# Performance work log

Measured on AMD Instinct MI355X. Metric: run time of the kernel, lower is better.

The kernel has to match this reference:

```python
import jax, jax.numpy as jnp
import numpy as np

B, SEQ, ST, DIN, DK, DV = 2, 4096, 128, 1024, 64, 64
T = SEQ + 2 * ST  # 4352, divisible by 8 -> no pad branch in original


def _l2norm(t):
    # matches torch F.normalize(p=2, dim=-1, eps=1e-12)
    return t / jnp.maximum(jnp.linalg.norm(t, axis=-1, keepdims=True), 1e-12)


def setup_inputs() -> dict:
    key = jax.random.key(0)
    ks = jax.random.split(key, 9)
    x = jax.random.normal(ks[0], (B, T, DIN), dtype=jnp.float32)
    w = 0.02
    Wq = jax.random.normal(ks[1], (DK, DIN), dtype=jnp.float32) * w
    Wk = jax.random.normal(ks[2], (DK, DIN), dtype=jnp.float32) * w
    Wv = jax.random.normal(ks[3], (DV, DIN), dtype=jnp.float32) * w
    Wq_s = jax.random.normal(ks[4], (DK, DIN), dtype=jnp.float32) * w
    Wk_s = jax.random.normal(ks[5], (DK, DIN), dtype=jnp.float32) * w
    Wv_s = jax.random.normal(ks[6], (DV, DIN), dtype=jnp.float32) * w
    cope_emb = jax.random.normal(ks[7], (DK, T), dtype=jnp.float32)  # (1, dim_key, seq_len+2*state_len) squeezed
    scale = jnp.array([0.125], dtype=jnp.float32)  # learnable scaling_factor param
    return {"x": x, "Wq": Wq, "Wk": Wk, "Wv": Wv, "Wq_s": Wq_s,
            "Wk_s": Wk_s, "Wv_s": Wv_s, "cope_emb": cope_emb, "scale": scale}


def reference(x, Wq, Wk, Wv, Wq_s, Wk_s, Wv_s, cope_emb, scale):
    # extract_state: start-state, sequence, end-state
    xs, xm, xe = x[:, :ST], x[:, ST:ST + SEQ], x[:, ST + SEQ:]
    # project (Linear, no bias) then L2-normalize each token vector
    q = jnp.concatenate([_l2norm(xs @ Wq_s.T), _l2norm(xm @ Wq.T), _l2norm(xe @ Wq_s.T)], axis=1)
    k = jnp.concatenate([_l2norm(xs @ Wk_s.T), _l2norm(xm @ Wk.T), _l2norm(xe @ Wk_s.T)], axis=1)
    v = jnp.concatenate([_l2norm(xs @ Wv_s.T), _l2norm(xm @ Wv.T), _l2norm(xe @ Wv_s.T)], axis=1)

    # q@k^T is used both for CoPE gates and (scaled) attention scores
    logits = jnp.einsum('btd,bsd->bts', q, k)  # (B, T, T)

    # --- CoPE bias ---
    gates = jax.nn.sigmoid(logits)
    pos = jnp.cumsum(gates[:, :, ::-1], axis=-1)[:, :, ::-1]  # flip-cumsum-flip
    pos = jnp.minimum(pos, jnp.float32(T - 1))
    pos_floor = jnp.floor(pos)
    pos_ceil = jnp.ceil(pos)
    w = pos - pos_floor
    logits_int = jnp.einsum('btd,dl->btl', q, cope_emb)  # (B, T, T)
    lc = jnp.take_along_axis(logits_int, pos_ceil.astype(jnp.int32), axis=-1)
    lf = jnp.take_along_axis(logits_int, pos_floor.astype(jnp.int32), axis=-1)
    cope_bias = lc * w + lf * (1.0 - w)

    # --- causal + state-token mask: tril, with end-state rows blocked from start-state cols ---
    i = jnp.arange(T)
    mask = i[:, None] >= i[None, :]
    blocked = (i[:, None] >= SEQ + ST) & (i[None, :] < ST)
    mask = mask & (~blocked)
    attn_bias = jnp.where(mask, 0.0, -jnp.inf)[None, :, :]

    scores = logits * scale[0] + attn_bias + cope_bias
    att = jax.nn.softmax(scores, axis=-1) @ v  # (B, T, DV)
    return att
```

## Files before the change

kernel.cpp:

```cpp
#include <hip/hip_runtime.h>
#include <math.h>

#define B_ 2
#define SEQ_ 4096
#define ST_ 128
#define T_ 4352
#define DIN_ 1024
#define NW 16
#define LMAX 3328
#define LPAD 3336
#define NSLICE 272
#define SLPAD 273
#define NROW 8704

typedef _Float16 f16;
typedef __attribute__((ext_vector_type(8))) _Float16 f16x8;
typedef __attribute__((ext_vector_type(4))) float f32x4;

#define OB_WH  0
#define OB_WL  786432
#define OB_QH  1572864
#define OB_QL  2686976
#define OB_KH  3801088
#define OB_KL  4915200
#define OB_VT  6029312
#define OB_CPT 7143424
#define OB_SS  7569408
#define OB_XH  17039360
#define OB_XL  34865152
#define NEED_NEW 52690944ull

#define WT4_OFF 0
#define Q_OFF   393216
#define KT_OFF  950272
#define V_OFF   1507328

__device__ __forceinline__ int wuid() {
  return __builtin_amdgcn_readfirstlane((int)(threadIdx.x >> 6));
}

template<int CTRL, int RM>
__device__ __forceinline__ float dppadd(float x) {
  int y = __builtin_amdgcn_update_dpp(0, __float_as_int(x), CTRL, RM, 0xf, true);
  return x + __int_as_float(y);
}
__device__ __forceinline__ float wave_iscan(float x) {
  x = dppadd<0x111, 0xf>(x);
  x = dppadd<0x112, 0xf>(x);
  x = dppadd<0x114, 0xf>(x);
  x = dppadd<0x118, 0xf>(x);
  x = dppadd<0x142, 0xa>(x);
  x = dppadd<0x143, 0xc>(x);
  return x;
}
__device__ __forceinline__ float p16scan(float x) {
  x = dppadd<0x111, 0xf>(x);
  x = dppadd<0x112, 0xf>(x);
  x = dppadd<0x114, 0xf>(x);
  x = dppadd<0x118, 0xf>(x);
  return x;
}
__device__ __forceinline__ float swz15(float x) {
  return __int_as_float(__builtin_amdgcn_ds_swizzle(__float_as_int(x), 0x1F0));
}

__global__ __launch_bounds__(256) void wsplit_kernel(
    const float* __restrict__ Wq,  const float* __restrict__ Wk,
    const float* __restrict__ Wv,  const float* __restrict__ Wqs,
    const float* __restrict__ Wks, const float* __restrict__ Wvs,
    f16* __restrict__ wh, f16* __restrict__ wl) {
  const int m = blockIdx.y;
  const float* src = (m==0)?Wq:(m==1)?Wqs:(m==2)?Wk:(m==3)?Wks:(m==4)?Wv:Wvs;
  const int g0 = (int)blockIdx.x * 4096 + (int)threadIdx.x * 16;
  const float4* s4 = reinterpret_cast<const float4*>(src + g0);
  float4 v0 = s4[0], v1 = s4[1], v2 = s4[2], v3 = s4[3];
  f16x8 h0, h1, l0, l1;
  h0[0]=(f16)v0.x; h0[1]=(f16)v0.y; h0[2]=(f16)v0.z; h0[3]=(f16)v0.w;
  h0[4]=(f16)v1.x; h0[5]=(f16)v1.y; h0[6]=(f16)v1.z; h0[7]=(f16)v1.w;
  h1[0]=(f16)v2.x; h1[1]=(f16)v2.y; h1[2]=(f16)v2.z; h1[3]=(f16)v2.w;
  h1[4]=(f16)v3.x; h1[5]=(f16)v3.y; h1[6]=(f16)v3.z; h1[7]=(f16)v3.w;
  l0[0]=(f16)(v0.x-(float)h0[0]); l0[1]=(f16)(v0.y-(float)h0[1]);
  l0[2]=(f16)(v0.z-(float)h0[2]); l0[3]=(f16)(v0.w-(float)h0[3]);
  l0[4]=(f16)(v1.x-(float)h0[4]); l0[5]=(f16)(v1.y-(float)h0[5]);
  l0[6]=(f16)(v1.z-(float)h0[6]); l0[7]=(f16)(v1.w-(float)h0[7]);
  l1[0]=(f16)(v2.x-(float)h1[0]); l1[1]=(f16)(v2.y-(float)h1[1]);
  l1[2]=(f16)(v2.z-(float)h1[2]); l1[3]=(f16)(v2.w-(float)h1[3]);
  l1[4]=(f16)(v3.x-(float)h1[4]); l1[5]=(f16)(v3.y-(float)h1[5]);
  l1[6]=(f16)(v3.z-(float)h1[6]); l1[7]=(f16)(v3.w-(float)h1[7]);
  const size_t o = (size_t)m * 65536 + g0;
  *reinterpret_cast<f16x8*>(wh + o) = h0;
  *reinterpret_cast<f16x8*>(wh + o + 8) = h1;
  *reinterpret_cast<f16x8*>(wl + o) = l0;
  *reinterpret_cast<f16x8*>(wl + o + 8) = l1;
}

__global__ __launch_bounds__(256) void xsplit_kernel(
    const float* __restrict__ x, f16* __restrict__ xh, f16* __restrict__ xl) {
  const size_t g0 = ((size_t)blockIdx.x * 256 + threadIdx.x) * 16;
  const float4* s4 = reinterpret_cast<const float4*>(x + g0);
  float4 v0 = s4[0], v1 = s4[1], v2 = s4[2], v3 = s4[3];
  f16x8 h0, h1, l0, l1;
  h0[0]=(f16)v0.x; h0[1]=(f16)v0.y; h0[2]=(f16)v0.z; h0[3]=(f16)v0.w;
  h0[4]=(f16)v1.x; h0[5]=(f16)v1.y; h0[6]=(f16)v1.z; h0[7]=(f16)v1.w;
  h1[0]=(f16)v2.x; h1[1]=(f16)v2.y; h1[2]=(f16)v2.z; h1[3]=(f16)v2.w;
  h1[4]=(f16)v3.x; h1[5]=(f16)v3.y; h1[6]=(f16)v3.z; h1[7]=(f16)v3.w;
  l0[0]=(f16)(v0.x-(float)h0[0]); l0[1]=(f16)(v0.y-(float)h0[1]);
  l0[2]=(f16)(v0.z-(float)h0[2]); l0[3]=(f16)(v0.w-(float)h0[3]);
  l0[4]=(f16)(v1.x-(float)h0[4]); l0[5]=(f16)(v1.y-(float)h0[5]);
  l0[6]=(f16)(v1.z-(float)h0[6]); l0[7]=(f16)(v1.w-(float)h0[7]);
  l1[0]=(f16)(v2.x-(float)h1[0]); l1[1]=(f16)(v2.y-(float)h1[1]);
  l1[2]=(f16)(v2.z-(float)h1[2]); l1[3]=(f16)(v2.w-(float)h1[3]);
  l1[4]=(f16)(v3.x-(float)h1[4]); l1[5]=(f16)(v3.y-(float)h1[5]);
  l1[6]=(f16)(v3.z-(float)h1[6]); l1[7]=(f16)(v3.w-(float)h1[7]);
  *reinterpret_cast<f16x8*>(xh + g0) = h0;
  *reinterpret_cast<f16x8*>(xh + g0 + 8) = h1;
  *reinterpret_cast<f16x8*>(xl + g0) = l0;
  *reinterpret_cast<f16x8*>(xl + g0 + 8) = l1;
}

__global__ __launch_bounds__(256) void copet_kernel(
    const float* __restrict__ cope, f16* __restrict__ copeT) {
  __shared__ float t2[64][65];
  const int l0 = blockIdx.x << 6;
  const int tid = (int)threadIdx.x;
  #pragma unroll
  for (int p = 0; p < 16; ++p) {
    int d = (p << 2) + (tid >> 6), c = tid & 63;
    t2[d][c] = cope[(size_t)d * T_ + l0 + c];
  }
  __syncthreads();
  #pragma unroll
  for (int p = 0; p < 16; ++p) {
    int l = (p << 2) + (tid >> 6), d = tid & 63;
    copeT[(size_t)(l0 + l) * 64 + d] = (f16)t2[d][l];
  }
}

#define PM_MFMA(ACC, WHP, WLP) { \
  f16x8 bh_ = *reinterpret_cast<const f16x8*>((WHP) + (st << 5)); \
  f16x8 bl_ = *reinterpret_cast<const f16x8*>((WLP) + (st << 5)); \
  ACC = __builtin_amdgcn_mfma_f32_16x16x32_f16(xh_, bh_, ACC, 0, 0, 0); \
  ACC = __builtin_amdgcn_mfma_f32_16x16x32_f16(xl_, bh_, ACC, 0, 0, 0); \
  ACC = __builtin_amdgcn_mfma_f32_16x16x32_f16(xh_, bl_, ACC, 0, 0, 0); }

#define PM_RED(ACC, P) { \
  float s0_ = ACC[0]*ACC[0], s1_ = ACC[1]*ACC[1], s2_ = ACC[2]*ACC[2], s3_ = ACC[3]*ACC[3]; \
  s0_ += __shfl_xor(s0_, 1, 64); s1_ += __shfl_xor(s1_, 1, 64); \
  s2_ += __shfl_xor(s2_, 1, 64); s3_ += __shfl_xor(s3_, 1, 64); \
  s0_ += __shfl_xor(s0_, 2, 64); s1_ += __shfl_xor(s1_, 2, 64); \
  s2_ += __shfl_xor(s2_, 2, 64); s3_ += __shfl_xor(s3_, 2, 64); \
  s0_ += __shfl_xor(s0_, 4, 64); s1_ += __shfl_xor(s1_, 4, 64); \
  s2_ += __shfl_xor(s2_, 4, 64); s3_ += __shfl_xor(s3_, 4, 64); \
  s0_ += __shfl_xor(s0_, 8, 64); s1_ += __shfl_xor(s1_, 8, 64); \
  s2_ += __shfl_xor(s2_, 8, 64); s3_ += __shfl_xor(s3_, 8, 64); \
  if (qlo == 0) { \
    ssq[wn][P][(qhi << 2) + 0] = s0_; ssq[wn][P][(qhi << 2) + 1] = s1_; \
    ssq[wn][P][(qhi << 2) + 2] = s2_; ssq[wn][P][(qhi << 2) + 3] = s3_; } }

#define PM_QK1(ACC, P, HH, LL, RG) { \
  float tt_ = ssq[0][P][(qhi << 2) + RG] + ssq[1][P][(qhi << 2) + RG] \
            + ssq[2][P][(qhi << 2) + RG] + ssq[3][P][(qhi << 2) + RG]; \
  float rn_ = 1.f / fmaxf(sqrtf(tt_), 1e-12f); \
  float v_ = ACC[RG] * rn_; \
  f16 h_ = (f16)v_; \
  size_t ad_ = (size_t)(bt0 + (qhi << 2) + RG) * 64 + (wn << 4) + qlo; \
  HH[ad_] = h_; LL[ad_] = (f16)(v_ - (float)h_); }

#define PM_V1(ACC, P, RG) { \
  float tt_ = ssq[0][P][(qhi << 2) + RG] + ssq[1][P][(qhi << 2) + RG] \
            + ssq[2][P][(qhi << 2) + RG] + ssq[3][P][(qhi << 2) + RG]; \
  float rn_ = 1.f / fmaxf(sqrtf(tt_), 1e-12f); \
  vt[(size_t)(b * 64 + (wn << 4) + qlo) * T_ + t0 + (qhi << 2) + RG] = (f16)(ACC[RG] * rn_); }

__global__ __launch_bounds__(512, 4) void projM_kernel(
    const f16* __restrict__ xh, const f16* __restrict__ xl,
    const f16* __restrict__ wh, const f16* __restrict__ wl,
    f16* __restrict__ qh, f16* __restrict__ ql,
    f16* __restrict__ kh, f16* __restrict__ kl,
    f16* __restrict__ vt) {
  __shared__ float ssq[4][3][16];
  __shared__ float part[4][64][12];
  const int lane = (int)threadIdx.x & 63;
  const int w = wuid();
  const int wn = w & 3;
  const int kh2 = w >> 2;
  const int qlo = lane & 15, qhi = lane >> 4;
  const int bt0 = (int)blockIdx.x << 4;
  const int b = bt0 / T_;
  const int t0 = bt0 - b * T_;
  const int spec = (t0 < ST_ || t0 >= ST_ + SEQ_) ? 1 : 0;

  const int kof = kh2 << 9;
  const f16* xhr = xh + (size_t)(bt0 + qlo) * DIN_ + kof + (qhi << 3);
  const f16* xlr = xl + (size_t)(bt0 + qlo) * DIN_ + kof + (qhi << 3);
  const size_t wrow = (size_t)((wn << 4) + qlo) * 1024 + kof + (qhi << 3);
  const f16* wq  = wh + (size_t)(0 + spec) * 65536 + wrow;
  const f16* wqL = wl + (size_t)(0 + spec) * 65536 + wrow;
  const f16* wk  = wh + (size_t)(2 + spec) * 65536 + wrow;
  const f16* wkL = wl + (size_t)(2 + spec) * 65536 + wrow;
  const f16* wv  = wh + (size_t)(4 + spec) * 65536 + wrow;
  const f16* wvL = wl + (size_t)(4 + spec) * 65536 + wrow;

  f32x4 aq = {0.f,0.f,0.f,0.f}, ak = {0.f,0.f,0.f,0.f}, av = {0.f,0.f,0.f,0.f};

  #pragma unroll 4
  for (int st = 0; st < 16; ++st) {
    f16x8 xh_ = *reinterpret_cast<const f16x8*>(xhr + (st << 5));
    f16x8 xl_ = *reinterpret_cast<const f16x8*>(xlr + (st << 5));
    PM_MFMA(aq, wq, wqL)
    PM_MFMA(ak, wk, wkL)
    PM_MFMA(av, wv, wvL)
  }

  if (w >= 4) {
    float* p = &part[w - 4][lane][0];
    p[0] = aq[0]; p[1] = aq[1]; p[2]  = aq[2]; p[3]  = aq[3];
    p[4] = ak[0]; p[5] = ak[1]; p[6]  = ak[2]; p[7]  = ak[3];
    p[8] = av[0]; p[9] = av[1]; p[10] = av[2]; p[11] = av[3];
  }
  __syncthreads();
  if (w < 4) {
    const float* p = &part[w][lane][0];
    aq[0] += p[0]; aq[1] += p[1]; aq[2] += p[2];  aq[3] += p[3];
    ak[0] += p[4]; ak[1] += p[5]; ak[2] += p[6];  ak[3] += p[7];
    av[0] += p[8]; av[1] += p[9]; av[2] += p[10]; av[3] += p[11];
    PM_RED(aq, 0) PM_RED(ak, 1) PM_RED(av, 2)
  }
  __syncthreads();
  if (w < 4) {
    PM_QK1(aq, 0, qh, ql, 0) PM_QK1(aq, 0, qh, ql, 1)
    PM_QK1(aq, 0, qh, ql, 2) PM_QK1(aq, 0, qh, ql, 3)
    PM_QK1(ak, 1, kh, kl, 0) PM_QK1(ak, 1, kh, kl, 1)
    PM_QK1(ak, 1, kh, kl, 2) PM_QK1(ak, 1, kh, kl, 3)
    PM_V1(av, 2, 0) PM_V1(av, 2, 1) PM_V1(av, 2, 2) PM_V1(av, 2, 3)
  }
}

#define QKD(SF, NF) { \
  int sg_ = swb + (NF << 4) + qlo; \
  int scl_ = sg_ < T_ ? sg_ : T_ - 1; \
  const f16* krh_ = kh + bT64 + (size_t)scl_ * 64 + (qhi << 3); \
  f16x8 bh0_ = *reinterpret_cast<const f16x8*>(krh_); \
  f16x8 bh1_ = *reinterpret_cast<const f16x8*>(krh_ + 32); \
  f32x4 a_ = {0.f, 0.f, 0.f, 0.f}; \
  a_ = __builtin_amdgcn_mfma_f32_16x16x32_f16(aqh0, bh0_, a_, 0, 0, 0); \
  a_ = __builtin_amdgcn_mfma_f32_16x16x32_f16(aqh1, bh1_, a_, 0, 0, 0); \
  SF = a_; }

#define PXA(SF, RG, SSV, LF, LC, WF) { \
  float g_ = 1.f / (1.f + __expf(-SF[RG])); \
  float in_ = p16scan(g_); \
  float pos_ = SSV - in_ + g_; \
  pos_ = pos_ < 0.f ? 0.f : (pos_ > 3326.f ? 3326.f : pos_); \
  int idx_ = (int)pos_; \
  WF = pos_ - (float)idx_; \
  const f16* lrow_ = liL + ((qhi << 2) + RG) * LPAD + idx_; \
  LF = (float)lrow_[0]; LC = (float)lrow_[1]; }

#define PXB(SF, NF, RG, LF, LC, WF) { \
  int sg_ = swb + (NF << 4) + qlo; \
  float bias_ = fmaf(WF, LC - LF, LF); \
  int tl_ = t0 + (qhi << 2) + RG; \
  bool valid_ = (sg_ <= tl_) && !((tl_ >= ST_ + SEQ_) && (sg_ < ST_)); \
  float p_ = valid_ ? __expf(fmaf(SF[RG], sc, bias_) - mrw[RG]) : 0.f; \
  lsum[RG] += p_; \
  pst[((qhi << 2) + RG) * 40 + (NF << 4) + qlo] = (f16)p_; }

#define PVF(OA, NF) { \
  int d_ = (NF << 4) + qlo; \
  const f16* vr_ = vt + (size_t)(b * 64 + d_) * T_; \
  f16x8 v0_ = *reinterpret_cast<const f16x8*>(vr_ + sv0); \
  OA = __builtin_amdgcn_mfma_f32_16x16x32_f16(pa0, v0_, OA, 0, 0, 0); }

#define OST(OA, NF) { \
  ob[w * 1024 + ((qhi << 2) + 0) * 64 + (NF << 4) + qlo] = OA[0]; \
  ob[w * 1024 + ((qhi << 2) + 1) * 64 + (NF << 4) + qlo] = OA[1]; \
  ob[w * 1024 + ((qhi << 2) + 2) * 64 + (NF << 4) + qlo] = OA[2]; \
  ob[w * 1024 + ((qhi << 2) + 3) * 64 + (NF << 4) + qlo] = OA[3]; }

__global__ __launch_bounds__(1024, 4) void attnE_kernel(
    const f16* __restrict__ qh, const f16* __restrict__ kh,
    const f16* __restrict__ vt, const f16* __restrict__ cpt,
    const float* __restrict__ scalep, float* __restrict__ out) {
  __shared__ __align__(16) f16 liL[16 * LPAD];
  __shared__ __align__(16) f16 pstage[NW * 16 * 40];
  __shared__ float sl[16][SLPAD];
  __shared__ float totF[NW][16];
  __shared__ float rmxS[NW][16];

  const int tid = (int)threadIdx.x;
  const int lane = tid & 63;
  const int w = wuid();
  const int bt0 = ((int)(gridDim.x - 1 - blockIdx.x)) << 4;
  const int b = bt0 / T_;
  const int t0 = bt0 - b * T_;
  const float sc = scalep[0];
  const int qlo = lane & 15, qhi = lane >> 4;

  const f16* qrp = qh + (size_t)(bt0 + qlo) * 64 + (qhi << 3);
  f16x8 aqh0 = *reinterpret_cast<const f16x8*>(qrp);
  f16x8 aqh1 = *reinterpret_cast<const f16x8*>(qrp + 32);
  const size_t bT64 = (size_t)(b * T_) * 64;

  {
    f32x4 rm = {-1e30f, -1e30f, -1e30f, -1e30f};
    #pragma unroll 2
    for (int c = 0; c < 13; ++c) {
      const int lf = w * 208 + (c << 4);
      const f16* cr = cpt + (size_t)(lf + qlo) * 64 + (qhi << 3);
      f16x8 b0 = *reinterpret_cast<const f16x8*>(cr);
      f16x8 b1 = *reinterpret_cast<const f16x8*>(cr + 32);
      f32x4 a = {0.f, 0.f, 0.f, 0.f};
      a = __builtin_amdgcn_mfma_f32_16x16x32_f16(aqh0, b0, a, 0, 0, 0);
      a = __builtin_amdgcn_mfma_f32_16x16x32_f16(aqh1, b1, a, 0, 0, 0);
      f16 h0_ = (f16)a[0]; liL[((qhi << 2) + 0) * LPAD + lf + qlo] = h0_; rm[0] = fmaxf(rm[0], (float)h0_);
      f16 h1_ = (f16)a[1]; liL[((qhi << 2) + 1) * LPAD + lf + qlo] = h1_; rm[1] = fmaxf(rm[1], (float)h1_);
      f16 h2_ = (f16)a[2]; liL[((qhi << 2) + 2) * LPAD + lf + qlo] = h2_; rm[2] = fmaxf(rm[2], (float)h2_);
      f16 h3_ = (f16)a[3]; liL[((qhi << 2) + 3) * LPAD + lf + qlo] = h3_; rm[3] = fmaxf(rm[3], (float)h3_);
    }
    #pragma unroll
    for (int k = 1; k < 16; k <<= 1) {
      rm[0] = fmaxf(rm[0], __shfl_xor(rm[0], k, 64));
      rm[1] = fmaxf(rm[1], __shfl_xor(rm[1], k, 64));
      rm[2] = fmaxf(rm[2], __shfl_xor(rm[2], k, 64));
      rm[3] = fmaxf(rm[3], __shfl_xor(rm[3], k, 64));
    }
    if (qlo == 0) {
      rmxS[w][(qhi << 2) + 0] = rm[0];
      rmxS[w][(qhi << 2) + 1] = rm[1];
      rmxS[w][(qhi << 2) + 2] = rm[2];
      rmxS[w][(qhi << 2) + 3] = rm[3];
    }
  }

  for (int i = 0; i < 17; ++i) {
    const int sli = w * 17 + i;
    const int sg = (sli << 4) + qlo;
    const f16* krh_ = kh + bT64 + (size_t)sg * 64 + (qhi << 3);
    f16x8 bh0 = *reinterpret_cast<const f16x8*>(krh_);
    f16x8 bh1 = *reinterpret_cast<const f16x8*>(krh_ + 32);
    f32x4 a = {0.f, 0.f, 0.f, 0.f};
    a = __builtin_amdgcn_mfma_f32_16x16x32_f16(aqh0, bh0, a, 0, 0, 0);
    a = __builtin_amdgcn_mfma_f32_16x16x32_f16(aqh1, bh1, a, 0, 0, 0);
    float g0 = 1.f / (1.f + __expf(-a[0])); float s0 = p16scan(g0);
    float g1 = 1.f / (1.f + __expf(-a[1])); float s1 = p16scan(g1);
    float g2 = 1.f / (1.f + __expf(-a[2])); float s2 = p16scan(g2);
    float g3 = 1.f / (1.f + __expf(-a[3])); float s3 = p16scan(g3);
    if (qlo == 15) {
      sl[(qhi << 2) + 0][sli] = s0;
      sl[(qhi << 2) + 1][sli] = s1;
      sl[(qhi << 2) + 2][sli] = s2;
      sl[(qhi << 2) + 3][sli] = s3;
    }
  }
  __syncthreads();

  {
    const int row = w;
    float* r = &sl[row][0];
    const int base = NSLICE - 1 - 5 * lane;
    double v0 = 0.0, v1 = 0.0, v2 = 0.0, v3 = 0.0, v4 = 0.0;
    double acc = 0.0;
    if (base - 0 >= 0) { acc += (double)r[base - 0]; } v0 = acc;
    if (base - 1 >= 0) { acc += (double)r[base - 1]; } v1 = acc;
    if (base - 2 >= 0) { acc += (double)r[base - 2]; } v2 = acc;
    if (base - 3 >= 0) { acc += (double)r[base - 3]; } v3 = acc;
    if (base - 4 >= 0) { acc += (double)r[base - 4]; } v4 = acc;
    double x = acc;
    #pragma unroll
    for (int off = 1; off < 64; off <<= 1) {
      double y = __shfl_up(x, off, 64);
      if (lane >= off) x += y;
    }
    const double offn = x - acc;
    if (base - 0 >= 0) r[base - 0] = (float)(v0 + offn);
    if (base - 1 >= 0) r[base - 1] = (float)(v1 + offn);
    if (base - 2 >= 0) r[base - 2] = (float)(v2 + offn);
    if (base - 3 >= 0) r[base - 3] = (float)(v3 + offn);
    if (base - 4 >= 0) r[base - 4] = (float)(v4 + offn);
  }

  f32x4 mrw;
  #pragma unroll
  for (int reg = 0; reg < 4; ++reg) {
    float mm = rmxS[0][(qhi << 2) + reg];
    #pragma unroll
    for (int w2 = 1; w2 < NW; ++w2) mm = fmaxf(mm, rmxS[w2][(qhi << 2) + reg]);
    mrw[reg] = mm + fabsf(sc) + 2e-3f;
  }
  __syncthreads();

  f16* pst = pstage + w * 640;

  f32x4 o0 = {0.f,0.f,0.f,0.f}, o1 = {0.f,0.f,0.f,0.f};
  f32x4 o2 = {0.f,0.f,0.f,0.f}, o3 = {0.f,0.f,0.f,0.f};
  f32x4 lsum = {0.f,0.f,0.f,0.f};

  const int jtmax = (t0 + 15) >> 9;
  for (int jt = jtmax; jt >= 0; --jt) {
    const int swb = (jt << 9) + (w << 5);
    f32x4 sf0, sf1;
    QKD(sf0, 0) QKD(sf1, 1)
    const int sbr = swb >> 4;
    const int sb0 = sbr < (NSLICE - 1) ? sbr : (NSLICE - 1);
    const int sb1 = (sbr + 1) < (NSLICE - 1) ? (sbr + 1) : (NSLICE - 1);
    float sA0 = sl[(qhi << 2) + 0][sb0];
    float sA1 = sl[(qhi << 2) + 1][sb0];
    float sA2 = sl[(qhi << 2) + 2][sb0];
    float sA3 = sl[(qhi << 2) + 3][sb0];
    float sB0 = sl[(qhi << 2) + 0][sb1];
    float sB1 = sl[(qhi << 2) + 1][sb1];
    float sB2 = sl[(qhi << 2) + 2][sb1];
    float sB3 = sl[(qhi << 2) + 3][sb1];
    float lf0, lc0, wf0, lf1, lc1, wf1, lf2, lc2, wf2, lf3, lc3, wf3;
    float lf4, lc4, wf4, lf5, lc5, wf5, lf6, lc6, wf6, lf7, lc7, wf7;
    PXA(sf0, 0, sA0, lf0, lc0, wf0) PXA(sf0, 1, sA1, lf1, lc1, wf1)
    PXA(sf0, 2, sA2, lf2, lc2, wf2) PXA(sf0, 3, sA3, lf3, lc3, wf3)
    PXA(sf1, 0, sB0, lf4, lc4, wf4) PXA(sf1, 1, sB1, lf5, lc5, wf5)
    PXA(sf1, 2, sB2, lf6, lc6, wf6) PXA(sf1, 3, sB3, lf7, lc7, wf7)
    PXB(sf0, 0, 0, lf0, lc0, wf0) PXB(sf0, 0, 1, lf1, lc1, wf1)
    PXB(sf0, 0, 2, lf2, lc2, wf2) PXB(sf0, 0, 3, lf3, lc3, wf3)
    PXB(sf1, 1, 0, lf4, lc4, wf4) PXB(sf1, 1, 1, lf5, lc5, wf5)
    PXB(sf1, 1, 2, lf6, lc6, wf6) PXB(sf1, 1, 3, lf7, lc7, wf7)
    {
      const f16* pr = pst + qlo * 40;
      f16x8 pa0 = *reinterpret_cast<const f16x8*>(pr + (qhi << 3));
      int sv0 = swb + (qhi << 3);
      sv0 = sv0 < T_ - 8 ? sv0 : T_ - 8;
      PVF(o0, 0) PVF(o1, 1) PVF(o2, 2) PVF(o3, 3)
    }
  }

  #pragma unroll
  for (int k = 1; k < 16; k <<= 1) {
    lsum[0] += __shfl_xor(lsum[0], k, 64);
    lsum[1] += __shfl_xor(lsum[1], k, 64);
    lsum[2] += __shfl_xor(lsum[2], k, 64);
    lsum[3] += __shfl_xor(lsum[3], k, 64);
  }
  __syncthreads();
  if (qlo == 0) {
    totF[w][(qhi << 2) + 0] = lsum[0];
    totF[w][(qhi << 2) + 1] = lsum[1];
    totF[w][(qhi << 2) + 2] = lsum[2];
    totF[w][(qhi << 2) + 3] = lsum[3];
  }
  float* ob = reinterpret_cast<float*>(liL);
  OST(o0, 0) OST(o1, 1) OST(o2, 2) OST(o3, 3)
  __syncthreads();
  {
    const int r = tid >> 6, d = tid & 63;
    float L = 0.f, o = 0.f;
    #pragma unroll
    for (int w2 = 0; w2 < NW; ++w2) {
      L += totF[w2][r];
      o += ob[w2 * 1024 + tid];
    }
    out[(size_t)(bt0 + r) * 64 + d] = o / L;
  }
}

__global__ __launch_bounds__(256) void wtrans_kernel(
    const float* __restrict__ Wq,  const float* __restrict__ Wk,
    const float* __restrict__ Wv,  const float* __restrict__ Wqs,
    const float* __restrict__ Wks, const float* __restrict__ Wvs,
    float* __restrict__ ws) {
  const int m = blockIdx.y;
  const float* src = (m==0)?Wq:(m==1)?Wqs:(m==2)?Wk:(m==3)?Wks:(m==4)?Wv:Wvs;
  float* dst = ws + (size_t)m * (DIN_*64);
  const int bx = blockIdx.x;
  #pragma unroll
  for (int p = 0; p < 16; ++p) {
    int e = (int)threadIdx.x + (p << 8);
    int c = e & 3, o = (e >> 2) & 63;
    int i = (bx << 6) + (p << 2) + c;
    dst[(((bx << 4) + p) * 64 + o) * 4 + c] = src[o * DIN_ + i];
  }
}

__global__ __launch_bounds__(256) void proj_kernel(
    const float* __restrict__ x, float* __restrict__ ws) {
  __shared__ float tile[32][65];
  const int t0 = blockIdx.x << 5;
  const int b  = blockIdx.y;
  const int pj = blockIdx.z;
  const int spec = (t0 < ST_ || t0 >= ST_ + SEQ_) ? 1 : 0;
  const float4* W4 = reinterpret_cast<const float4*>(ws + WT4_OFF + (size_t)(pj*2 + spec) * (DIN_*64));
  const int lane = (int)threadIdx.x & 63;
  const int w = wuid();
  const float* xb = x + ((size_t)(b * T_ + t0 + (w << 3))) * DIN_;
  float acc[8] = {0.f,0.f,0.f,0.f,0.f,0.f,0.f,0.f};
  #pragma unroll 4
  for (int i4 = 0; i4 < 256; ++i4) {
    float4 wv = W4[(i4 << 6) + lane];
    #pragma unroll
    for (int r = 0; r < 8; ++r) {
      float4 xv = reinterpret_cast<const float4*>(xb + r * DIN_)[i4];
      acc[r] = fmaf(wv.x, xv.x, fmaf(wv.y, xv.y, fmaf(wv.z, xv.z, fmaf(wv.w, xv.w, acc[r]))));
    }
  }
  float outv[8];
  #pragma unroll
  for (int r = 0; r < 8; ++r) {
    float sq = acc[r] * acc[r];
    #pragma unroll
    for (int off = 32; off; off >>= 1) sq += __shfl_xor(sq, off, 64);
    float n = fmaxf(sqrtf(sq), 1e-12f);
    outv[r] = acc[r] / n;
  }
  const int trow = t0 + (w << 3);
  if (pj != 1) {
    float* dst = ws + (pj == 0 ? Q_OFF : V_OFF) + ((size_t)(b * T_ + trow)) * 64;
    #pragma unroll
    for (int r = 0; r < 8; ++r) dst[r * 64 + lane] = outv[r];
  } else {
    #pragma unroll
    for (int r = 0; r < 8; ++r) tile[(w << 3) + r][lane] = outv[r];
    __syncthreads();
    float* kt = ws + KT_OFF + (size_t)b * 16 * T_ * 4;
    #pragma unroll
    for (int p = 0; p < 8; ++p) {
      int e = (int)threadIdx.x + (p << 8);
      int c = e & 3, tt = (e >> 2) & 31, d4 = e >> 7;
      kt[((size_t)d4 * T_ + t0 + tt) * 4 + c] = tile[tt][(d4 << 2) + c];
    }
  }
}

__global__ __launch_bounds__(1024) void attn_kernel(
    const float* __restrict__ ws_c, const float* __restrict__ cope,
    const float* __restrict__ scalep, float* __restrict__ out) {
  __shared__ float li_s[8 * T_];
  __shared__ float pbuf[NW][8][32];
  __shared__ float totF[NW][8];
  __shared__ double suffD[NW][8];
  __shared__ double carryD[2][8];
  __shared__ float mlL[NW][8];
  __shared__ float wmax[NW][8];
  const int tid = (int)threadIdx.x;
  const int lane = tid & 63;
  const int w = wuid();
  const int t0 = ((int)(gridDim.x - 1 - blockIdx.x)) << 3;
  const int b  = blockIdx.y;
  const float* qrow = ws_c + Q_OFF + ((size_t)(b * T_ + t0)) * 64;
  const float* ktb  = ws_c + KT_OFF + (size_t)b * 16 * T_ * 4;
  const float* vb   = ws_c + V_OFF + ((size_t)b * T_) * 64;
  const float sc = scalep[0];
  if (tid < 8) carryD[0][tid] = 0.0;
  float lm[8];
  #pragma unroll
  for (int r = 0; r < 8; ++r) lm[r] = -INFINITY;
  for (int jt = 0; jt < 5; ++jt) {
    const int l = (jt << 10) + tid;
    if (l < T_) {
      float a[8] = {0,0,0,0,0,0,0,0};
      #pragma unroll 4
      for (int d4 = 0; d4 < 16; ++d4) {
        float c0 = cope[(d4 * 4 + 0) * T_ + l];
        float c1 = cope[(d4 * 4 + 1) * T_ + l];
        float c2 = cope[(d4 * 4 + 2) * T_ + l];
        float c3 = cope[(d4 * 4 + 3) * T_ + l];
        #pragma unroll
        for (int r = 0; r < 8; ++r) {
          float4 qq = *reinterpret_cast<const float4*>(qrow + r * 64 + (d4 << 2));
          a[r] = fmaf(c0, qq.x, fmaf(c1, qq.y, fmaf(c2, qq.z, fmaf(c3, qq.w, a[r]))));
        }
      }
      #pragma unroll
      for (int r = 0; r < 8; ++r) { li_s[r * T_ + l] = a[r]; lm[r] = fmaxf(lm[r], a[r]); }
    }
  }
  #pragma unroll
  for (int r = 0; r < 8; ++r) {
    #pragma unroll
    for (int off = 32; off; off >>= 1) lm[r] = fmaxf(lm[r], __shfl_xor(lm[r], off, 64));
  }
  if (lane == 0) {
    #pragma unroll
    for (int r = 0; r < 8; ++r) wmax[w][r] = lm[r];
  }
  __syncthreads();
  float mrow[8];
  #pragma unroll
  for (int r = 0; r < 8; ++r) {
    float mm = wmax[0][r];
    #pragma unroll
    for (int w2 = 1; w2 < NW; ++w2) mm = fmaxf(mm, wmax[w2][r]);
    mrow[r] = mm + fabsf(sc) + 1e-3f;
  }
  float acc[8]  = {0,0,0,0,0,0,0,0};
  float lsum[8] = {0,0,0,0,0,0,0,0};
  int par = 0;
  for (int jt = 4; jt >= 0; --jt) {
    const int s = (jt << 10) + tid;
    const bool sval = (s < T_);
    float lg[8] = {0,0,0,0,0,0,0,0};
    if (sval) {
      #pragma unroll 4
      for (int d4 = 0; d4 < 16; ++d4) {
        float4 kk = *reinterpret_cast<const float4*>(ktb + ((size_t)d4 * T_ + s) * 4);
        #pragma unroll
        for (int r = 0; r < 8; ++r) {
          float4 qq = *reinterpret_cast<const float4*>(qrow + r * 64 + (d4 << 2));
          lg[r] = fmaf(kk.x, qq.x, fmaf(kk.y, qq.y, fmaf(kk.z, qq.z, fmaf(kk.w, qq.w, lg[r]))));
        }
      }
    }
    float locsuf[8], gtot[8];
    #pragma unroll
    for (int r = 0; r < 8; ++r) {
      float g = sval ? 1.f / (1.f + __expf(-lg[r])) : 0.f;
      float xx = wave_iscan(g);
      float tt = __shfl(xx, 63, 64);
      locsuf[r] = tt - xx + g;
      gtot[r] = tt;
    }
    if (lane == 0) {
      #pragma unroll
      for (int r = 0; r < 8; ++r) totF[w][r] = gtot[r];
    }
    __syncthreads();
    if (tid < 128) {
      const int w2 = tid >> 3, r = tid & 7;
      float ssum = 0.f;
      for (int w3 = w2 + 1; w3 < NW; ++w3) ssum += totF[w3][r];
      suffD[w2][r] = carryD[par][r] + (double)ssum;
      if (w2 == 0) carryD[par ^ 1][r] = carryD[par][r] + (double)(ssum + totF[0][r]);
    }
    __syncthreads();
    par ^= 1;
    if ((jt << 10) > t0 + 7) continue;
    float p[8];
    #pragma unroll
    for (int r = 0; r < 8; ++r) {
      double posd = suffD[w][r] + (double)locsuf[r];
      if (posd > 4351.0) posd = 4351.0;
      int idx = (int)posd;
      float wf = (float)(posd - (double)idx);
      int idx2 = idx < 4351 ? idx + 1 : 4351;
      float lf = li_s[r * T_ + idx];
      float lc = li_s[r * T_ + idx2];
      float bias = fmaf(wf, lc - lf, lf);
      const int t = t0 + r;
      const bool valid = sval && (s <= t) && !((t >= ST_ + SEQ_) && (s < ST_));
      float score = valid ? fmaf(lg[r], sc, bias) : -INFINITY;
      p[r] = __expf(score - mrow[r]);
      lsum[r] += p[r];
    }
    const int sbase = (jt << 10) + (w << 6);
    if (sbase < T_) {
      #pragma unroll
      for (int pass = 0; pass < 2; ++pass) {
        if ((lane >> 5) == pass) {
          #pragma unroll
          for (int r = 0; r < 8; ++r) pbuf[w][r][lane & 31] = p[r];
        }
        const int s0 = sbase + (pass << 5);
        #pragma unroll 4
        for (int s4 = 0; s4 < 8; ++s4) {
          const int sb = s0 + (s4 << 2);
          float v0 = vb[(size_t)(sb + 0) * 64 + lane];
          float v1 = vb[(size_t)(sb + 1) * 64 + lane];
          float v2 = vb[(size_t)(sb + 2) * 64 + lane];
          float v3 = vb[(size_t)(sb + 3) * 64 + lane];
          #pragma unroll
          for (int r = 0; r < 8; ++r) {
            float4 pr = *reinterpret_cast<const float4*>(&pbuf[w][r][s4 << 2]);
            acc[r] = fmaf(pr.x, v0, fmaf(pr.y, v1, fmaf(pr.z, v2, fmaf(pr.w, v3, acc[r]))));
          }
        }
      }
    }
  }
  #pragma unroll
  for (int r = 0; r < 8; ++r) {
    #pragma unroll
    for (int off = 32; off; off >>= 1) lsum[r] += __shfl_xor(lsum[r], off, 64);
  }
  if (lane == 0) {
    #pragma unroll
    for (int r = 0; r < 8; ++r) mlL[w][r] = lsum[r];
  }
  float* pb = &pbuf[w][0][0];
  #pragma unroll
  for (int pass = 0; pass < 2; ++pass) {
    __syncthreads();
    #pragma unroll
    for (int rr = 0; rr < 4; ++rr) pb[rr * 64 + lane] = acc[pass * 4 + rr];
    __syncthreads();
    if (tid < 256) {
      const int rr = tid >> 6, d = tid & 63;
      const int r = pass * 4 + rr;
      float o = 0.f, L = 0.f;
      #pragma unroll
      for (int w2 = 0; w2 < NW; ++w2) {
        o += (&pbuf[w2][0][0])[rr * 64 + d];
        L += mlL[w2][r];
      }
      out[((size_t)(b * T_ + t0 + r)) * 64 + d] = o / L;
    }
  }
}

extern "C" void kernel_launch(void* const* d_in, const int* in_sizes, int n_in,
                              void* d_out, int out_size, void* d_ws, size_t ws_size,
                              hipStream_t stream) {
  const float* x    = (const float*)d_in[0];
  const float* Wq   = (const float*)d_in[1];
  const float* Wk   = (const float*)d_in[2];
  const float* Wv   = (const float*)d_in[3];
  const float* Wqs  = (const float*)d_in[4];
  const float* Wks  = (const float*)d_in[5];
  const float* Wvs  = (const float*)d_in[6];
  const float* cope = (const float*)d_in[7];
  const float* scl  = (const float*)d_in[8];
  float* outp = (float*)d_out;
  (void)in_sizes; (void)n_in; (void)out_size;

  if (ws_size >= NEED_NEW) {
    unsigned char* wb = (unsigned char*)d_ws;
    f16* whp = (f16*)(wb + OB_WH);
    f16* wlp = (f16*)(wb + OB_WL);
    f16* qh = (f16*)(wb + OB_QH);
    f16* ql = (f16*)(wb + OB_QL);
    f16* kh = (f16*)(wb + OB_KH);
    f16* kl = (f16*)(wb + OB_KL);
    f16* vt = (f16*)(wb + OB_VT);
    f16* cpt = (f16*)(wb + OB_CPT);
    f16* xhp = (f16*)(wb + OB_XH);
    f16* xlp = (f16*)(wb + OB_XL);
    hipLaunchKernelGGL(wsplit_kernel, dim3(16, 6), dim3(256), 0, stream,
                       Wq, Wk, Wv, Wqs, Wks, Wvs, whp, wlp);
    hipLaunchKernelGGL(xsplit_kernel, dim3(2176), dim3(256), 0, stream, x, xhp, xlp);
    hipLaunchKernelGGL(copet_kernel, dim3(52), dim3(256), 0, stream, cope, cpt);
    hipLaunchKernelGGL(projM_kernel, dim3(544), dim3(512), 0, stream,
                       xhp, xlp, whp, wlp, qh, ql, kh, kl, vt);
    hipLaunchKernelGGL(attnE_kernel, dim3(544), dim3(1024), 0, stream,
                       qh, kh, vt, cpt, scl, outp);
  } else {
    float* ws = (float*)d_ws;
    hipLaunchKernelGGL(wtrans_kernel, dim3(16, 6), dim3(256), 0, stream,
                       Wq, Wk, Wv, Wqs, Wks, Wvs, ws);
    hipLaunchKernelGGL(proj_kernel, dim3(136, 2, 3), dim3(256), 0, stream, x, ws);
    hipLaunchKernelGGL(attn_kernel, dim3(544, 2), dim3(1024), 0, stream, ws, cope, scl, outp);
  }
}
```

Measured before the change: 250.9 us.

## Fuse x hi/lo split into projection and merge prep kernels

Removes the separate xsplit kernel, so projM now reads fp32 x directly and splits it into f16 hi/lo in registers. This avoids writing and re-reading about 35 MB of intermediate data. The weight-split and cope-transpose kernels are merged into one launch, and the unused q/k low-part writes are dropped. In exchange, projM does more conversion ALU work and its x loads are twice as wide, and its unroll factor drops from 4 to 2.

After: 236.8 us. 1.06x faster.

```diff
diff --git a/kernel.cpp b/kernel.cpp
--- a/kernel.cpp
+++ b/kernel.cpp
@@ -11,7 +11,6 @@
 #define LPAD 3336
 #define NSLICE 272
 #define SLPAD 273
-#define NROW 8704
 
 typedef _Float16 f16;
 typedef __attribute__((ext_vector_type(8))) _Float16 f16x8;
@@ -20,15 +19,10 @@
 #define OB_WH  0
 #define OB_WL  786432
 #define OB_QH  1572864
-#define OB_QL  2686976
-#define OB_KH  3801088
-#define OB_KL  4915200
-#define OB_VT  6029312
-#define OB_CPT 7143424
-#define OB_SS  7569408
-#define OB_XH  17039360
-#define OB_XL  34865152
-#define NEED_NEW 52690944ull
+#define OB_KH  2686976
+#define OB_VT  3801088
+#define OB_CPT 4915200
+#define NEED_NEW 5341184ull
 
 #define WT4_OFF 0
 #define Q_OFF   393216
@@ -64,75 +58,52 @@
   return __int_as_float(__builtin_amdgcn_ds_swizzle(__float_as_int(x), 0x1F0));
 }
 
-__global__ __launch_bounds__(256) void wsplit_kernel(
+__global__ __launch_bounds__(256) void prep_kernel(
     const float* __restrict__ Wq,  const float* __restrict__ Wk,
     const float* __restrict__ Wv,  const float* __restrict__ Wqs,
     const float* __restrict__ Wks, const float* __restrict__ Wvs,
-    f16* __restrict__ wh, f16* __restrict__ wl) {
-  const int m = blockIdx.y;
-  const float* src = (m==0)?Wq:(m==1)?Wqs:(m==2)?Wk:(m==3)?Wks:(m==4)?Wv:Wvs;
-  const int g0 = (int)blockIdx.x * 4096 + (int)threadIdx.x * 16;
-  const float4* s4 = reinterpret_cast<const float4*>(src + g0);
-  float4 v0 = s4[0], v1 = s4[1], v2 = s4[2], v3 = s4[3];
-  f16x8 h0, h1, l0, l1;
-  h0[0]=(f16)v0.x; h0[1]=(f16)v0.y; h0[2]=(f16)v0.z; h0[3]=(f16)v0.w;
-  h0[4]=(f16)v1.x; h0[5]=(f16)v1.y; h0[6]=(f16)v1.z; h0[7]=(f16)v1.w;
-  h1[0]=(f16)v2.x; h1[1]=(f16)v2.y; h1[2]=(f16)v2.z; h1[3]=(f16)v2.w;
-  h1[4]=(f16)v3.x; h1[5]=(f16)v3.y; h1[6]=(f16)v3.z; h1[7]=(f16)v3.w;
-  l0[0]=(f16)(v0.x-(float)h0[0]); l0[1]=(f16)(v0.y-(float)h0[1]);
-  l0[2]=(f16)(v0.z-(float)h0[2]); l0[3]=(f16)(v0.w-(float)h0[3]);
-  l0[4]=(f16)(v1.x-(float)h0[4]); l0[5]=(f16)(v1.y-(float)h0[5]);
-  l0[6]=(f16)(v1.z-(float)h0[6]); l0[7]=(f16)(v1.w-(float)h0[7]);
-  l1[0]=(f16)(v2.x-(float)h1[0]); l1[1]=(f16)(v2.y-(float)h1[1]);
-  l1[2]=(f16)(v2.z-(float)h1[2]); l1[3]=(f16)(v2.w-(float)h1[3]);
-  l1[4]=(f16)(v3.x-(float)h1[4]); l1[5]=(f16)(v3.y-(float)h1[5]);
-  l1[6]=(f16)(v3.z-(float)h1[6]); l1[7]=(f16)(v3.w-(float)h1[7]);
-  const size_t o = (size_t)m * 65536 + g0;
-  *reinterpret_cast<f16x8*>(wh + o) = h0;
-  *reinterpret_cast<f16x8*>(wh + o + 8) = h1;
-  *reinterpret_cast<f16x8*>(wl + o) = l0;
-  *reinterpret_cast<f16x8*>(wl + o + 8) = l1;
-}
-
-__global__ __launch_bounds__(256) void xsplit_kernel(
-    const float* __restrict__ x, f16* __restrict__ xh, f16* __restrict__ xl) {
-  const size_t g0 = ((size_t)blockIdx.x * 256 + threadIdx.x) * 16;
-  const float4* s4 = reinterpret_cast<const float4*>(x + g0);
-  float4 v0 = s4[0], v1 = s4[1], v2 = s4[2], v3 = s4[3];
-  f16x8 h0, h1, l0, l1;
-  h0[0]=(f16)v0.x; h0[1]=(f16)v0.y; h0[2]=(f16)v0.z; h0[3]=(f16)v0.w;
-  h0[4]=(f16)v1.x; h0[5]=(f16)v1.y; h0[6]=(f16)v1.z; h0[7]=(f16)v1.w;
-  h1[0]=(f16)v2.x; h1[1]=(f16)v2.y; h1[2]=(f16)v2.z; h1[3]=(f16)v2.w;
-  h1[4]=(f16)v3.x; h1[5]=(f16)v3.y; h1[6]=(f16)v3.z; h1[7]=(f16)v3.w;
-  l0[0]=(f16)(v0.x-(float)h0[0]); l0[1]=(f16)(v0.y-(float)h0[1]);
-  l0[2]=(f16)(v0.z-(float)h0[2]); l0[3]=(f16)(v0.w-(float)h0[3]);
-  l0[4]=(f16)(v1.x-(float)h0[4]); l0[5]=(f16)(v1.y-(float)h0[5]);
-  l0[6]=(f16)(v1.z-(float)h0[6]); l0[7]=(f16)(v1.w-(float)h0[7]);
-  l1[0]=(f16)(v2.x-(float)h1[0]); l1[1]=(f16)(v2.y-(float)h1[1]);
-  l1[2]=(f16)(v2.z-(float)h1[2]); l1[3]=(f16)(v2.w-(float)h1[3]);
-  l1[4]=(f16)(v3.x-(float)h1[4]); l1[5]=(f16)(v3.y-(float)h1[5]);
-  l1[6]=(f16)(v3.z-(float)h1[6]); l1[7]=(f16)(v3.w-(float)h1[7]);
-  *reinterpret_cast<f16x8*>(xh + g0) = h0;
-  *reinterpret_cast<f16x8*>(xh + g0 + 8) = h1;
-  *reinterpret_cast<f16x8*>(xl + g0) = l0;
-  *reinterpret_cast<f16x8*>(xl + g0 + 8) = l1;
-}
-
-__global__ __launch_bounds__(256) void copet_kernel(
-    const float* __restrict__ cope, f16* __restrict__ copeT) {
+    const float* __restrict__ cope,
+    f16* __restrict__ wh, f16* __restrict__ wl, f16* __restrict__ copeT) {
   __shared__ float t2[64][65];
-  const int l0 = blockIdx.x << 6;
+  const int id = (int)blockIdx.x;
   const int tid = (int)threadIdx.x;
-  #pragma unroll
-  for (int p = 0; p < 16; ++p) {
-    int d = (p << 2) + (tid >> 6), c = tid & 63;
-    t2[d][c] = cope[(size_t)d * T_ + l0 + c];
-  }
-  __syncthreads();
-  #pragma unroll
-  for (int p = 0; p < 16; ++p) {
-    int l = (p << 2) + (tid >> 6), d = tid & 63;
-    copeT[(size_t)(l0 + l) * 64 + d] = (f16)t2[d][l];
+  if (id < 96) {
+    const int m = id >> 4;
+    const float* src = (m==0)?Wq:(m==1)?Wqs:(m==2)?Wk:(m==3)?Wks:(m==4)?Wv:Wvs;
+    const int g0 = (id & 15) * 4096 + tid * 16;
+    const float4* s4 = reinterpret_cast<const float4*>(src + g0);
+    float4 v0 = s4[0], v1 = s4[1], v2 = s4[2], v3 = s4[3];
+    f16x8 h0, h1, l0, l1;
+    h0[0]=(f16)v0.x; h0[1]=(f16)v0.y; h0[2]=(f16)v0.z; h0[3]=(f16)v0.w;
+    h0[4]=(f16)v1.x; h0[5]=(f16)v1.y; h0[6]=(f16)v1.z; h0[7]=(f16)v1.w;
+    h1[0]=(f16)v2.x; h1[1]=(f16)v2.y; h1[2]=(f16)v2.z; h1[3]=(f16)v2.w;
+    h1[4]=(f16)v3.x; h1[5]=(f16)v3.y; h1[6]=(f16)v3.z; h1[7]=(f16)v3.w;
+    l0[0]=(f16)(v0.x-(float)h0[0]); l0[1]=(f16)(v0.y-(float)h0[1]);
+    l0[2]=(f16)(v0.z-(float)h0[2]); l0[3]=(f16)(v0.w-(float)h0[3]);
+    l0[4]=(f16)(v1.x-(float)h0[4]); l0[5]=(f16)(v1.y-(float)h0[5]);
+    l0[6]=(f16)(v1.z-(float)h0[6]); l0[7]=(f16)(v1.w-(float)h0[7]);
+    l1[0]=(f16)(v2.x-(float)h1[0]); l1[1]=(f16)(v2.y-(float)h1[1]);
+    l1[2]=(f16)(v2.z-(float)h1[2]); l1[3]=(f16)(v2.w-(float)h1[3]);
+    l1[4]=(f16)(v3.x-(float)h1[4]); l1[5]=(f16)(v3.y-(float)h1[5]);
+    l1[6]=(f16)(v3.z-(float)h1[6]); l1[7]=(f16)(v3.w-(float)h1[7]);
+    const size_t o = (size_t)m * 65536 + g0;
+    *reinterpret_cast<f16x8*>(wh + o) = h0;
+    *reinterpret_cast<f16x8*>(wh + o + 8) = h1;
+    *reinterpret_cast<f16x8*>(wl + o) = l0;
+    *reinterpret_cast<f16x8*>(wl + o + 8) = l1;
+  } else {
+    const int l0i = (id - 96) << 6;
+    #pragma unroll
+    for (int p = 0; p < 16; ++p) {
+      int d = (p << 2) + (tid >> 6), c = tid & 63;
+      t2[d][c] = cope[(size_t)d * T_ + l0i + c];
+    }
+    __syncthreads();
+    #pragma unroll
+    for (int p = 0; p < 16; ++p) {
+      int l = (p << 2) + (tid >> 6), d = tid & 63;
+      copeT[(size_t)(l0i + l) * 64 + d] = (f16)t2[d][l];
+    }
   }
 }
 
@@ -157,14 +128,12 @@
     ssq[wn][P][(qhi << 2) + 0] = s0_; ssq[wn][P][(qhi << 2) + 1] = s1_; \
     ssq[wn][P][(qhi << 2) + 2] = s2_; ssq[wn][P][(qhi << 2) + 3] = s3_; } }
 
-#define PM_QK1(ACC, P, HH, LL, RG) { \
+#define PM_QK1(ACC, P, HH, RG) { \
   float tt_ = ssq[0][P][(qhi << 2) + RG] + ssq[1][P][(qhi << 2) + RG] \
             + ssq[2][P][(qhi << 2) + RG] + ssq[3][P][(qhi << 2) + RG]; \
   float rn_ = 1.f / fmaxf(sqrtf(tt_), 1e-12f); \
   float v_ = ACC[RG] * rn_; \
-  f16 h_ = (f16)v_; \
-  size_t ad_ = (size_t)(bt0 + (qhi << 2) + RG) * 64 + (wn << 4) + qlo; \
-  HH[ad_] = h_; LL[ad_] = (f16)(v_ - (float)h_); }
+  HH[(size_t)(bt0 + (qhi << 2) + RG) * 64 + (wn << 4) + qlo] = (f16)v_; }
 
 #define PM_V1(ACC, P, RG) { \
   float tt_ = ssq[0][P][(qhi << 2) + RG] + ssq[1][P][(qhi << 2) + RG] \
@@ -173,11 +142,9 @@
   vt[(size_t)(b * 64 + (wn << 4) + qlo) * T_ + t0 + (qhi << 2) + RG] = (f16)(ACC[RG] * rn_); }
 
 __global__ __launch_bounds__(512, 4) void projM_kernel(
-    const f16* __restrict__ xh, const f16* __restrict__ xl,
+    const float* __restrict__ x,
     const f16* __restrict__ wh, const f16* __restrict__ wl,
-    f16* __restrict__ qh, f16* __restrict__ ql,
-    f16* __restrict__ kh, f16* __restrict__ kl,
-    f16* __restrict__ vt) {
+    f16* __restrict__ qh, f16* __restrict__ kh, f16* __restrict__ vt) {
   __shared__ float ssq[4][3][16];
   __shared__ float part[4][64][12];
   const int lane = (int)threadIdx.x & 63;
@@ -191,8 +158,7 @@
   const int spec = (t0 < ST_ || t0 >= ST_ + SEQ_) ? 1 : 0;
 
   const int kof = kh2 << 9;
-  const f16* xhr = xh + (size_t)(bt0 + qlo) * DIN_ + kof + (qhi << 3);
-  const f16* xlr = xl + (size_t)(bt0 + qlo) * DIN_ + kof + (qhi << 3);
+  const float* xr = x + (size_t)(bt0 + qlo) * DIN_ + kof + (qhi << 3);
   const size_t wrow = (size_t)((wn << 4) + qlo) * 1024 + kof + (qhi << 3);
   const f16* wq  = wh + (size_t)(0 + spec) * 65536 + wrow;
   const f16* wqL = wl + (size_t)(0 + spec) * 65536 + wrow;
@@ -203,10 +169,17 @@
 
   f32x4 aq = {0.f,0.f,0.f,0.f}, ak = {0.f,0.f,0.f,0.f}, av = {0.f,0.f,0.f,0.f};
 
-  #pragma unroll 4
+  #pragma unroll 2
   for (int st = 0; st < 16; ++st) {
-    f16x8 xh_ = *reinterpret_cast<const f16x8*>(xhr + (st << 5));
-    f16x8 xl_ = *reinterpret_cast<const f16x8*>(xlr + (st << 5));
+    float4 xa_ = *reinterpret_cast<const float4*>(xr + (st << 5));
+    float4 xb_ = *reinterpret_cast<const float4*>(xr + (st << 5) + 4);
+    f16x8 xh_, xl_;
+    xh_[0]=(f16)xa_.x; xh_[1]=(f16)xa_.y; xh_[2]=(f16)xa_.z; xh_[3]=(f16)xa_.w;
+    xh_[4]=(f16)xb_.x; xh_[5]=(f16)xb_.y; xh_[6]=(f16)xb_.z; xh_[7]=(f16)xb_.w;
+    xl_[0]=(f16)(xa_.x-(float)xh_[0]); xl_[1]=(f16)(xa_.y-(float)xh_[1]);
+    xl_[2]=(f16)(xa_.z-(float)xh_[2]); xl_[3]=(f16)(xa_.w-(float)xh_[3]);
+    xl_[4]=(f16)(xb_.x-(float)xh_[4]); xl_[5]=(f16)(xb_.y-(float)xh_[5]);
+    xl_[6]=(f16)(xb_.z-(float)xh_[6]); xl_[7]=(f16)(xb_.w-(float)xh_[7]);
     PM_MFMA(aq, wq, wqL)
     PM_MFMA(ak, wk, wkL)
     PM_MFMA(av, wv, wvL)
@@ -228,10 +201,10 @@
   }
   __syncthreads();
   if (w < 4) {
-    PM_QK1(aq, 0, qh, ql, 0) PM_QK1(aq, 0, qh, ql, 1)
-    PM_QK1(aq, 0, qh, ql, 2) PM_QK1(aq, 0, qh, ql, 3)
-    PM_QK1(ak, 1, kh, kl, 0) PM_QK1(ak, 1, kh, kl, 1)
-    PM_QK1(ak, 1, kh, kl, 2) PM_QK1(ak, 1, kh, kl, 3)
+    PM_QK1(aq, 0, qh, 0) PM_QK1(aq, 0, qh, 1)
+    PM_QK1(aq, 0, qh, 2) PM_QK1(aq, 0, qh, 3)
+    PM_QK1(ak, 1, kh, 0) PM_QK1(ak, 1, kh, 1)
+    PM_QK1(ak, 1, kh, 2) PM_QK1(ak, 1, kh, 3)
     PM_V1(av, 2, 0) PM_V1(av, 2, 1) PM_V1(av, 2, 2) PM_V1(av, 2, 3)
   }
 }
@@ -356,8 +329,7 @@
   __syncthreads();
 
   {
-    const int row = w;
-    float* r = &sl[row][0];
+    float* r = &sl[w][0];
     const int base = NSLICE - 1 - 5 * lane;
     double v0 = 0.0, v1 = 0.0, v2 = 0.0, v3 = 0.0, v4 = 0.0;
     double acc = 0.0;
@@ -722,19 +694,13 @@
     f16* whp = (f16*)(wb + OB_WH);
     f16* wlp = (f16*)(wb + OB_WL);
     f16* qh = (f16*)(wb + OB_QH);
-    f16* ql = (f16*)(wb + OB_QL);
     f16* kh = (f16*)(wb + OB_KH);
-    f16* kl = (f16*)(wb + OB_KL);
     f16* vt = (f16*)(wb + OB_VT);
     f16* cpt = (f16*)(wb + OB_CPT);
-    f16* xhp = (f16*)(wb + OB_XH);
-    f16* xlp = (f16*)(wb + OB_XL);
-    hipLaunchKernelGGL(wsplit_kernel, dim3(16, 6), dim3(256), 0, stream,
-                       Wq, Wk, Wv, Wqs, Wks, Wvs, whp, wlp);
-    hipLaunchKernelGGL(xsplit_kernel, dim3(2176), dim3(256), 0, stream, x, xhp, xlp);
-    hipLaunchKernelGGL(copet_kernel, dim3(52), dim3(256), 0, stream, cope, cpt);
+    hipLaunchKernelGGL(prep_kernel, dim3(148), dim3(256), 0, stream,
+                       Wq, Wk, Wv, Wqs, Wks, Wvs, cope, whp, wlp, cpt);
     hipLaunchKernelGGL(projM_kernel, dim3(544), dim3(512), 0, stream,
-                       xhp, xlp, whp, wlp, qh, ql, kh, kl, vt);
+                       x, whp, wlp, qh, kh, vt);
     hipLaunchKernelGGL(attnE_kernel, dim3(544), dim3(1024), 0, stream,
                        qh, kh, vt, cpt, scl, outp);
   } else {
```
